# Optimization experiments

Hardware: AMD Instinct MI355X
Metric: run time of the kernel (lower is better)

Reference implementation:

```python
import jax, jax.numpy as jnp
import numpy as np

NUM_HEADS = 8
EPS = 1e-12  # torch F.normalize default eps


def conv1x1(x, w):
    # x: [b,c,h,w], w: [o,c]
    return jnp.einsum('bchw,oc->bohw', x, w)


def dwconv3x3(x, w):
    # depthwise 3x3, w: [c,1,3,3]
    return jax.lax.conv_general_dilated(
        x, w, window_strides=(1, 1), padding=((1, 1), (1, 1)),
        dimension_numbers=('NCHW', 'OIHW', 'NCHW'),
        feature_group_count=x.shape[1])


def l2norm(x):
    n = jnp.sqrt(jnp.sum(x * x, axis=-1, keepdims=True))
    return x / jnp.maximum(n, EPS)


def channel_attn(q, k, v, temperature, b, c, h, w):
    hd = c // NUM_HEADS
    q = l2norm(q.reshape(b, NUM_HEADS, hd, h * w))
    k = l2norm(k.reshape(b, NUM_HEADS, hd, h * w))
    v = v.reshape(b, NUM_HEADS, hd, h * w)
    attn = jnp.einsum('bndl,bnel->bnde', q, k) * temperature  # [b,nh,hd,hd]
    attn = jax.nn.softmax(attn, axis=-1)
    out = jnp.einsum('bnde,bnel->bndl', attn, v)
    return out.reshape(b, c, h, w)


def fdfp(x, w1, w2, h, w):
    xf = jnp.fft.rfft2(x, norm='ortho')  # over last two axes
    xfreq = jnp.concatenate([xf.real, xf.imag], axis=1)
    xfreq = conv1x1(xfreq, w1)
    xfreq = jax.nn.gelu(xfreq, approximate=False)
    xfreq = conv1x1(xfreq, w2)
    c2 = xfreq.shape[1] // 2
    xc = jax.lax.complex(xfreq[:, :c2], xfreq[:, c2:])
    return jnp.fft.irfft2(xc, s=(h, w), norm='ortho')


def setup_inputs() -> dict:
    key = jax.random.key(0)
    ks = jax.random.split(key, 10)
    dim = 192
    b, h, w = 4, 128, 128
    s = 0.05
    return {
        'x': jax.random.normal(ks[0], (b, dim, h, w), jnp.float32),
        'w_qkv1': jax.random.normal(ks[1], (3 * dim, dim), jnp.float32) * s,
        'w_qkv1_dw': jax.random.normal(ks[2], (3 * dim, 1, 3, 3), jnp.float32) * s,
        'w_proj1': jax.random.normal(ks[3], (dim, dim), jnp.float32) * s,
        'w_fdfp1': jax.random.normal(ks[4], (2 * dim, 2 * dim), jnp.float32) * s,
        'w_fdfp2': jax.random.normal(ks[5], (2 * dim, 2 * dim), jnp.float32) * s,
        'w_kv2': jax.random.normal(ks[6], (2 * dim, dim), jnp.float32) * s,
        'w_kv2_dw': jax.random.normal(ks[7], (2 * dim, 1, 3, 3), jnp.float32) * s,
        'w_proj2': jax.random.normal(ks[8], (dim, dim), jnp.float32) * s,
        'temperature': jnp.ones((NUM_HEADS, 1, 1), jnp.float32),
    }


def reference(x, w_qkv1, w_qkv1_dw, w_proj1, w_fdfp1, w_fdfp2,
              w_kv2, w_kv2_dw, w_proj2, temperature):
    b, c, h, w = x.shape
    # Stage 1: spatial-domain transposed (channel) attention
    qkv1 = dwconv3x3(conv1x1(x, w_qkv1), w_qkv1_dw)
    q1, k1, v1 = jnp.split(qkv1, 3, axis=1)
    out1 = channel_attn(q1, k1, v1, temperature, b, c, h, w)
    out1 = conv1x1(out1, w_proj1)
    # Stage 2: frequency-domain query, spatial K/V from stage-1 output
    q2 = fdfp(x, w_fdfp1, w_fdfp2, h, w)
    kv2 = dwconv3x3(conv1x1(out1, w_kv2), w_kv2_dw)
    k2, v2 = jnp.split(kv2, 2, axis=1)
    out2 = channel_attn(q2, k2, v2, temperature, b, c, h, w)
    out2 = conv1x1(out2, w_proj2)
    return out2
```

## Files before the change

kernel.cpp:

```cpp
#include <hip/hip_runtime.h>
#include <math.h>

typedef _Float16 half_t;
typedef half_t h8v __attribute__((ext_vector_type(8)));
typedef half_t h4v __attribute__((ext_vector_type(4)));
typedef float f32x4 __attribute__((ext_vector_type(4)));

namespace {
constexpr int DIMC = 192;
constexpr int NB = 4;
constexpr int HH = 128, WW = 128;
constexpr int HW = HH * WW;
constexpr int NH = 8, HD = 24;
constexpr int FP = 80;
constexpr long LT_PART = 128L * 192 * FP;
constexpr long LT_B    = 2 * LT_PART;
constexpr long LT_ROW  = 192L * FP;
constexpr long XB  = 192L * HW;
constexpr long CB0 = 0;
constexpr long CB1 = 15728640;
constexpr long OFF_T1 = 37748736;
constexpr long OFF_Q2 = 50331648;
constexpr long OFF_S  = 62914560;
constexpr long OFF_KT = 0;
constexpr long OFF_KF = 25165824;
constexpr long OFF_O2 = 0;
constexpr int  GSL = 64;
constexpr long SM_INVQ1 = OFF_S;
constexpr long SM_INVK1 = OFF_S + 768;
constexpr long SM_INVQ2 = OFF_S + 1536;
constexpr long SM_INVK2 = OFF_S + 2304;
constexpr long SM_ATT   = OFF_S + 3072;
constexpr long H0       = OFF_S + 168960;
constexpr long H_WQKV = H0;
constexpr long H_WF   = H0 + 55296;
constexpr long H_W1   = H0 + 92160;
constexpr long H_W2   = H0 + 165888;
constexpr long H_PRJ  = H0 + 239616;
constexpr long H_B2   = H0 + 258048;
constexpr long H_B3   = H0 + 290816;
constexpr long H_B1T  = H0 + 323584;
constexpr long H_B4T  = H0 + 333824;
constexpr float PI2 = 6.283185307179586476f;
}

__global__ void cvt16_k(const float* __restrict__ in, half_t* __restrict__ o, int n) {
    int i = blockIdx.x * 256 + threadIdx.x;
    if (i < n) o[i] = (half_t)in[i];
}
__global__ void initB1t_k(half_t* __restrict__ B) {
    int idx = blockIdx.x * 256 + threadIdx.x;
    if (idx >= 160 * 128) return;
    int j = idx / 128, k = idx % 128;
    float v = 0.f;
    if (j < 65) v = cosf(PI2 * ((k * j) & 127) / 128.f) * (1.f / 128.f);
    else if (j >= 80 && j < 145) v = -sinf(PI2 * ((k * (j - 80)) & 127) / 128.f) * (1.f / 128.f);
    B[idx] = (half_t)v;
}
__global__ void initB2h_k(half_t* __restrict__ B) {
    int idx = blockIdx.x * 256 + threadIdx.x;
    int m = idx >> 8, cin = idx & 255;
    int pd = m >> 7, ky = m & 127;
    int ps = cin >> 7, y = cin & 127;
    float c, s; sincosf(PI2 * ((ky * y) & 127) / 128.f, &s, &c);
    float v = (pd == 0) ? (ps == 0 ? c : s) : (ps == 0 ? -s : c);
    B[idx] = (half_t)v;
}
__global__ void initB3h_k(half_t* __restrict__ B) {
    int idx = blockIdx.x * 256 + threadIdx.x;
    int m = idx >> 8, cin = idx & 255;
    int pd = m >> 7, y = m & 127;
    int ps = cin >> 7, ky = cin & 127;
    float c, s; sincosf(PI2 * ((y * ky) & 127) / 128.f, &s, &c);
    float v = (pd == 0) ? (ps == 0 ? c : -s) : (ps == 0 ? s : c);
    B[idx] = (half_t)v;
}
__global__ void initB4t_k(half_t* __restrict__ B) {
    int idx = blockIdx.x * 256 + threadIdx.x;
    if (idx >= 128 * 160) return;
    int j = idx / 160, k = idx % 160;
    float v = 0.f;
    if (k < 80) {
        if (k == 0) v = 1.f / 128.f;
        else if (k < 64) v = 2.f * cosf(PI2 * ((k * j) & 127) / 128.f) / 128.f;
        else if (k == 64) v = cosf(PI2 * ((64 * j) & 127) / 128.f) / 128.f;
    } else {
        int kx = k - 80;
        if (kx >= 1 && kx < 64) v = -2.f * sinf(PI2 * ((kx * j) & 127) / 128.f) / 128.f;
    }
    B[idx] = (half_t)v;
}
__global__ void fusew_k(const float* __restrict__ wkv, const float* __restrict__ wproj,
                        half_t* __restrict__ wf) {
    int o = blockIdx.x, c = threadIdx.x;
    float acc = 0.f;
    for (int m = 0; m < 192; ++m) acc += wkv[o * 192 + m] * wproj[m * 192 + c];
    wf[o * 192 + c] = (half_t)acc;
}

template<int PFOLD, int GELU>
__global__ __launch_bounds__(256) void k2m(
    const half_t* __restrict__ W16, int Cin,
    const float* __restrict__ X, long xBatch, int iSplit, long iLo, long iHi,
    float* __restrict__ out, long oBatch, int oSplit, long oLo, long oHi) {
    __shared__ __align__(16) half_t Wh[64 * 40];
    __shared__ __align__(16) half_t Xh[256 * 40];
    const int t = threadIdx.x;
    const int o0 = blockIdx.x * 64;
    const long p0 = (long)blockIdx.y * 256;
    const long xb = (long)blockIdx.z * xBatch;
    const long ob = (long)blockIdx.z * oBatch;
    const int lane = t & 63, wv = t >> 6;
    const int fr = lane & 15, fg = lane >> 4;
    const int so = t >> 2, scg = (t & 3) * 8;
    f32x4 acc[4][4];
#pragma unroll
    for (int m = 0; m < 4; ++m)
#pragma unroll
        for (int n = 0; n < 4; ++n) acc[m][n] = {0.f, 0.f, 0.f, 0.f};
    long pa;
    {
        long p = p0 + t;
        if (PFOLD) { long q = p / 80; pa = q * LT_ROW + (p - q * 80); } else pa = p;
    }
    for (int k0 = 0; k0 < Cin; k0 += 32) {
        __syncthreads();
        *(h8v*)&Wh[so * 40 + scg] =
            *(const h8v*)(W16 + (long)(o0 + so) * Cin + k0 + scg);
#pragma unroll
        for (int s = 0; s < 2; ++s) {
            int cb = k0 + s * 16;
            long rb = (cb < iSplit) ? (long)cb * iLo : (long)(cb - iSplit) * iLo + iHi;
            const float* g = X + xb + rb + pa;
            float v[16];
#pragma unroll
            for (int j = 0; j < 16; ++j) v[j] = g[(long)j * iLo];
            h8v h0, h1;
#pragma unroll
            for (int j = 0; j < 8; ++j) { h0[j] = (half_t)v[j]; h1[j] = (half_t)v[8 + j]; }
            *(h8v*)&Xh[t * 40 + s * 16] = h0;
            *(h8v*)&Xh[t * 40 + s * 16 + 8] = h1;
        }
        __syncthreads();
        h8v a[4], bb[4];
#pragma unroll
        for (int m = 0; m < 4; ++m) a[m] = *(const h8v*)&Wh[(m * 16 + fr) * 40 + fg * 8];
#pragma unroll
        for (int n = 0; n < 4; ++n) bb[n] = *(const h8v*)&Xh[(wv * 64 + n * 16 + fr) * 40 + fg * 8];
#pragma unroll
        for (int m = 0; m < 4; ++m)
#pragma unroll
            for (int n = 0; n < 4; ++n)
                acc[m][n] = __builtin_amdgcn_mfma_f32_16x16x32_f16(a[m], bb[n], acc[m][n], 0, 0, 0);
    }
    long pe[4];
#pragma unroll
    for (int n = 0; n < 4; ++n) {
        long p = p0 + wv * 64 + n * 16 + fr;
        if (PFOLD) { long q = p / 80; pe[n] = q * LT_ROW + (p - q * 80); } else pe[n] = p;
    }
#pragma unroll
    for (int m = 0; m < 4; ++m)
#pragma unroll
        for (int i = 0; i < 4; ++i) {
            int o = o0 + m * 16 + fg * 4 + i;
            long oadr = ob + ((o < oSplit) ? (long)o * oLo : (long)(o - oSplit) * oLo + oHi);
#pragma unroll
            for (int n = 0; n < 4; ++n) {
                float v = acc[m][n][i];
                if (GELU) v = 0.5f * v * (1.f + erff(v * 0.70710678118654752f));
                out[oadr + pe[n]] = v;
            }
        }
}

__global__ __launch_bounds__(256) void k2big(
    const half_t* __restrict__ B16,
    const float* __restrict__ X, float* __restrict__ out) {
    __shared__ __align__(16) half_t Xh[8 * 64 * 40];
    const int t = threadIdx.x;
    const long p0 = (long)blockIdx.x * 64;
    const long xb = (long)blockIdx.y * LT_B;
    const int lane = t & 63, wv = t >> 6;
    const int fr = lane & 15, fg = lane >> 4;
    {
        const int sp = t & 63;
        const int c0 = t >> 6;
        const float* gp = X + xb + p0 + sp;
#pragma unroll 8
        for (int j = 0; j < 64; ++j) {
            int ci = c0 + j * 4;
            long rb = (ci < 128) ? (long)ci * LT_ROW : (long)(ci - 128) * LT_ROW + LT_PART;
            Xh[((ci >> 5) * 64 + sp) * 40 + (ci & 31)] = (half_t)gp[rb];
        }
    }
    __syncthreads();
    f32x4 acc[4][4];
#pragma unroll
    for (int m = 0; m < 4; ++m)
#pragma unroll
        for (int n = 0; n < 4; ++n) acc[m][n] = {0.f, 0.f, 0.f, 0.f};
    for (int k0 = 0; k0 < 256; k0 += 32) {
        const int s = k0 >> 5;
        h8v a[4], bb[4];
#pragma unroll
        for (int m = 0; m < 4; ++m)
            a[m] = *(const h8v*)(B16 + (long)(wv * 64 + m * 16 + fr) * 256 + k0 + fg * 8);
#pragma unroll
        for (int n = 0; n < 4; ++n)
            bb[n] = *(const h8v*)&Xh[(s * 64 + n * 16 + fr) * 40 + fg * 8];
#pragma unroll
        for (int m = 0; m < 4; ++m)
#pragma unroll
            for (int n = 0; n < 4; ++n)
                acc[m][n] = __builtin_amdgcn_mfma_f32_16x16x32_f16(a[m], bb[n], acc[m][n], 0, 0, 0);
    }
#pragma unroll
    for (int m = 0; m < 4; ++m)
#pragma unroll
        for (int i = 0; i < 4; ++i) {
            int o = wv * 64 + m * 16 + fg * 4 + i;
            long oadr = xb + ((o < 128) ? (long)o * LT_ROW : (long)(o - 128) * LT_ROW + LT_PART);
#pragma unroll
            for (int n = 0; n < 4; ++n)
                out[oadr + p0 + n * 16 + fr] = acc[m][n][i];
        }
}

__global__ __launch_bounds__(512) void kff4(
    const half_t* __restrict__ W1, const half_t* __restrict__ W2,
    const float* __restrict__ X, float* __restrict__ out) {
    __shared__ __align__(16) half_t S[12 * 64 * 40];
    const int t = threadIdx.x;
    const long p0 = (long)blockIdx.x * 64;
    const long xb = (long)blockIdx.y * LT_B;
    const int lane = t & 63, wv = t >> 6;
    const int fr = lane & 15, fg = lane >> 4;
    {
        const int sp = t & 63;
        const int g = t >> 6;
        long pa; { long p = p0 + sp; long q = p / 80; pa = q * LT_ROW + (p - q * 80); }
        const float* gp = X + xb + pa;
#pragma unroll
        for (int ch = 0; ch < 12; ++ch) {
            int ci0 = ch * 32 + g * 4;
            h4v h;
#pragma unroll
            for (int j = 0; j < 4; ++j) {
                int ci = ci0 + j;
                long rb = (ci < 192) ? (long)ci * 80 : (long)(ci - 192) * 80 + LT_PART;
                h[j] = (half_t)gp[rb];
            }
            *(h4v*)&S[(ch * 64 + sp) * 40 + g * 4] = h;
        }
    }
    __syncthreads();
    f32x4 acc[3][4];
#pragma unroll
    for (int m = 0; m < 3; ++m)
#pragma unroll
        for (int n = 0; n < 4; ++n) acc[m][n] = {0.f, 0.f, 0.f, 0.f};
    for (int k0 = 0; k0 < 384; k0 += 32) {
        const int s = k0 >> 5;
        h8v a[3], bb[4];
#pragma unroll
        for (int m = 0; m < 3; ++m)
            a[m] = *(const h8v*)(W1 + (long)(wv * 48 + m * 16 + fr) * 384 + k0 + fg * 8);
#pragma unroll
        for (int n = 0; n < 4; ++n)
            bb[n] = *(const h8v*)&S[(s * 64 + n * 16 + fr) * 40 + fg * 8];
#pragma unroll
        for (int m = 0; m < 3; ++m)
#pragma unroll
            for (int n = 0; n < 4; ++n)
                acc[m][n] = __builtin_amdgcn_mfma_f32_16x16x32_f16(a[m], bb[n], acc[m][n], 0, 0, 0);
    }
    __syncthreads();
#pragma unroll
    for (int m = 0; m < 3; ++m)
#pragma unroll
        for (int n = 0; n < 4; ++n) {
            int o4 = wv * 48 + m * 16 + fg * 4;
            int p = n * 16 + fr;
            h4v h;
#pragma unroll
            for (int i = 0; i < 4; ++i) {
                float v = acc[m][n][i];
                v = 0.5f * v * (1.f + erff(v * 0.70710678118654752f));
                h[i] = (half_t)v;
            }
            *(h4v*)&S[((o4 >> 5) * 64 + p) * 40 + (o4 & 31)] = h;
        }
#pragma unroll
    for (int m = 0; m < 3; ++m)
#pragma unroll
        for (int n = 0; n < 4; ++n) acc[m][n] = {0.f, 0.f, 0.f, 0.f};
    __syncthreads();
    for (int k0 = 0; k0 < 384; k0 += 32) {
        const int s = k0 >> 5;
        h8v a[3], bb[4];
#pragma unroll
        for (int m = 0; m < 3; ++m)
            a[m] = *(const h8v*)(W2 + (long)(wv * 48 + m * 16 + fr) * 384 + k0 + fg * 8);
#pragma unroll
        for (int n = 0; n < 4; ++n)
            bb[n] = *(const h8v*)&S[(s * 64 + n * 16 + fr) * 40 + fg * 8];
#pragma unroll
        for (int m = 0; m < 3; ++m)
#pragma unroll
            for (int n = 0; n < 4; ++n)
                acc[m][n] = __builtin_amdgcn_mfma_f32_16x16x32_f16(a[m], bb[n], acc[m][n], 0, 0, 0);
    }
    long pe[4];
#pragma unroll
    for (int n = 0; n < 4; ++n) {
        long p = p0 + n * 16 + fr;
        long q = p / 80; pe[n] = q * LT_ROW + (p - q * 80);
    }
#pragma unroll
    for (int m = 0; m < 3; ++m)
#pragma unroll
        for (int i = 0; i < 4; ++i) {
            int o = wv * 48 + m * 16 + fg * 4 + i;
            long oadr = xb + ((o < 192) ? (long)o * 80 : (long)(o - 192) * 80 + LT_PART);
#pragma unroll
            for (int n = 0; n < 4; ++n) out[oadr + pe[n]] = acc[m][n][i];
        }
}

template<int NF, int NORM>
__global__ __launch_bounds__(256) void k1m(
    const float* __restrict__ A, long aBatch, long aC, long aRow, int aSplit, long aHiOff, int K,
    const uint* __restrict__ Bt32,
    float* __restrict__ out, long oBatch, long oC, long oRow, int oSplit, long oHiOff,
    float* __restrict__ inv) {
    __shared__ __align__(16) half_t Ah[128 * 40];
    __shared__ __align__(16) half_t Bh[160 * 40];
    const int t = threadIdx.x;
    const long ab = (long)blockIdx.z * aBatch + (long)blockIdx.x * aC;
    const long ob = (long)blockIdx.z * oBatch + (long)blockIdx.x * oC;
    const int N = NF * 32;
    const int lane = t & 63, wv = t >> 6;
    const int wm = wv >> 1, wn = wv & 1;
    const int fr = lane & 15, fg = lane >> 4;
    const int sr = t >> 1, shalf = t & 1;
    const int Kw = K >> 1;
    f32x4 acc[4][NF];
#pragma unroll
    for (int m = 0; m < 4; ++m)
#pragma unroll
        for (int n = 0; n < NF; ++n) acc[m][n] = {0.f, 0.f, 0.f, 0.f};
    for (int k0 = 0; k0 < K; k0 += 32) {
        __syncthreads();
        {
            int cb = k0 + shalf * 16;
            long rb = (cb < aSplit) ? (long)cb : (long)(cb - aSplit) + aHiOff;
            const float* g = A + ab + (long)sr * aRow + rb;
            float4 v0 = *(const float4*)g;
            float4 v1 = *(const float4*)(g + 4);
            float4 v2 = *(const float4*)(g + 8);
            float4 v3 = *(const float4*)(g + 12);
            h8v h0, h1;
            h0[0] = (half_t)v0.x; h0[1] = (half_t)v0.y; h0[2] = (half_t)v0.z; h0[3] = (half_t)v0.w;
            h0[4] = (half_t)v1.x; h0[5] = (half_t)v1.y; h0[6] = (half_t)v1.z; h0[7] = (half_t)v1.w;
            h1[0] = (half_t)v2.x; h1[1] = (half_t)v2.y; h1[2] = (half_t)v2.z; h1[3] = (half_t)v2.w;
            h1[4] = (half_t)v3.x; h1[5] = (half_t)v3.y; h1[6] = (half_t)v3.z; h1[7] = (half_t)v3.w;
            *(h8v*)&Ah[sr * 40 + shalf * 16] = h0;
            *(h8v*)&Ah[sr * 40 + shalf * 16 + 8] = h1;
        }
        for (int j = t; j < N * 16; j += 256) {
            int n = j >> 4, kw = j & 15;
            *(uint*)&Bh[n * 40 + kw * 2] = Bt32[(long)n * Kw + (k0 >> 1) + kw];
        }
        __syncthreads();
        h8v a[4], bb[NF];
#pragma unroll
        for (int m = 0; m < 4; ++m) a[m] = *(const h8v*)&Ah[(wm * 64 + m * 16 + fr) * 40 + fg * 8];
#pragma unroll
        for (int n = 0; n < NF; ++n) bb[n] = *(const h8v*)&Bh[(wn * NF * 16 + n * 16 + fr) * 40 + fg * 8];
#pragma unroll
        for (int m = 0; m < 4; ++m)
#pragma unroll
            for (int n = 0; n < NF; ++n)
                acc[m][n] = __builtin_amdgcn_mfma_f32_16x16x32_f16(a[m], bb[n], acc[m][n], 0, 0, 0);
    }
#pragma unroll
    for (int m = 0; m < 4; ++m)
#pragma unroll
        for (int i = 0; i < 4; ++i) {
            int r = wm * 64 + m * 16 + fg * 4 + i;
            float* orow = out + ob + (long)r * oRow;
#pragma unroll
            for (int n = 0; n < NF; ++n) {
                int j = wn * NF * 16 + n * 16 + fr;
                long jm = (j < oSplit) ? (long)j : (long)(j - oSplit) + oHiOff;
                orow[jm] = acc[m][n][i];
            }
        }
    if (NORM) {
        float ss = 0.f;
#pragma unroll
        for (int m = 0; m < 4; ++m)
#pragma unroll
            for (int n = 0; n < NF; ++n)
#pragma unroll
                for (int i = 0; i < 4; ++i) ss += acc[m][n][i] * acc[m][n][i];
        __syncthreads();
        float* red = (float*)Ah;
        red[t] = ss;
        __syncthreads();
        for (int st = 128; st > 0; st >>= 1) {
            if (t < st) red[t] += red[t + st];
            __syncthreads();
        }
        if (t == 0) inv[(long)blockIdx.z * 192 + blockIdx.x] = 1.f / fmaxf(sqrtf(red[0]), 1e-12f);
    }
}

__global__ __launch_bounds__(256) void dw3_k(
    const float* __restrict__ in, long inBatch,
    const float* __restrict__ w9,
    float* __restrict__ out, long outBatch,
    int normCnt, float* __restrict__ inv) {
    const int c = blockIdx.x, b = blockIdx.y;
    const int t = threadIdx.x;
    const float* ip = in + (long)b * inBatch + (long)c * HW;
    float* op = out + (long)b * outBatch + (long)c * HW;
    const float* wp = w9 + c * 9;
    const float w0 = wp[0], w1 = wp[1], w2 = wp[2];
    const float w3 = wp[3], w4 = wp[4], w5 = wp[5];
    const float w6 = wp[6], w7 = wp[7], w8 = wp[8];
    const int tx = t & 31;
    const int x0 = tx * 4;
    const int y0 = (t >> 5) * 16;
    const bool lx = (tx > 0), rx = (tx < 31);
    float Ar[6], Br[6], Cr[6];
#define LOADROW(Y, R) do { \
        const float* _p = ip + (Y) * 128 + x0; \
        float4 _v = *(const float4*)_p; \
        R[1] = _v.x; R[2] = _v.y; R[3] = _v.z; R[4] = _v.w; \
        R[0] = lx ? _p[-1] : 0.f; \
        R[5] = rx ? _p[4] : 0.f; } while (0)
    if (y0 == 0) { Ar[0]=Ar[1]=Ar[2]=Ar[3]=Ar[4]=Ar[5]=0.f; }
    else LOADROW(y0 - 1, Ar);
    LOADROW(y0, Br);
    float ss = 0.f;
#pragma unroll
    for (int i = 0; i < 16; ++i) {
        int y = y0 + i;
        if (y + 1 < 128) { LOADROW(y + 1, Cr); }
        else { Cr[0]=Cr[1]=Cr[2]=Cr[3]=Cr[4]=Cr[5]=0.f; }
        float o0 = Ar[0]*w0 + Ar[1]*w1 + Ar[2]*w2
                 + Br[0]*w3 + Br[1]*w4 + Br[2]*w5
                 + Cr[0]*w6 + Cr[1]*w7 + Cr[2]*w8;
        float o1 = Ar[1]*w0 + Ar[2]*w1 + Ar[3]*w2
                 + Br[1]*w3 + Br[2]*w4 + Br[3]*w5
                 + Cr[1]*w6 + Cr[2]*w7 + Cr[3]*w8;
        float o2 = Ar[2]*w0 + Ar[3]*w1 + Ar[4]*w2
                 + Br[2]*w3 + Br[3]*w4 + Br[4]*w5
                 + Cr[2]*w6 + Cr[3]*w7 + Cr[4]*w8;
        float o3 = Ar[3]*w0 + Ar[4]*w1 + Ar[5]*w2
                 + Br[3]*w3 + Br[4]*w4 + Br[5]*w5
                 + Cr[3]*w6 + Cr[4]*w7 + Cr[5]*w8;
        *(float4*)(op + y * 128 + x0) = make_float4(o0, o1, o2, o3);
        ss += o0*o0 + o1*o1 + o2*o2 + o3*o3;
#pragma unroll
        for (int j = 0; j < 6; ++j) { Ar[j] = Br[j]; Br[j] = Cr[j]; }
    }
#undef LOADROW
    if (normCnt > 0 && c < normCnt) {
        __shared__ float red[256];
        red[t] = ss;
        __syncthreads();
        for (int st = 128; st > 0; st >>= 1) {
            if (t < st) red[t] += red[t + st];
            __syncthreads();
        }
        if (t == 0) inv[(long)b * 192 + c] = 1.f / fmaxf(sqrtf(red[0]), 1e-12f);
    }
}

__global__ __launch_bounds__(576) void gramf_k(
    const float* __restrict__ q, long qB,
    const float* __restrict__ k, long kB,
    float* __restrict__ gp) {
    __shared__ float qs[HD][260];
    __shared__ float ks[HD][260];
    const int bn = blockIdx.x, ls = blockIdx.y;
    const int b = bn >> 3, n = bn & 7;
    const int t = threadIdx.x;
    const int l0 = ls * 256;
    const float* qp = q + (long)b * qB + (long)(n * HD) * HW + l0;
    const float* kp = k + (long)b * kB + (long)(n * HD) * HW + l0;
    for (int idx = t; idx < HD * 64; idx += 576) {
        int row = idx >> 6, c4 = (idx & 63) * 4;
        *(float4*)&qs[row][c4] = *(const float4*)(qp + (long)row * HW + c4);
        *(float4*)&ks[row][c4] = *(const float4*)(kp + (long)row * HW + c4);
    }
    __syncthreads();
    const int d = t / 24, e = t - d * 24;
    float acc = 0.f;
#pragma unroll 8
    for (int j = 0; j < 256; j += 4) {
        float4 a = *(const float4*)&qs[d][j];
        float4 bb = *(const float4*)&ks[e][j];
        acc += a.x * bb.x + a.y * bb.y + a.z * bb.z + a.w * bb.w;
    }
    gp[((long)bn * 576 + t) * GSL + ls] = acc;
}

__global__ __launch_bounds__(256) void softmax_k(
    const float* __restrict__ gp, const float* __restrict__ invq,
    const float* __restrict__ invk, const float* __restrict__ temp,
    float* __restrict__ attn) {
    int bn = blockIdx.x;
    int b = bn >> 3, n = bn & 7;
    int t = threadIdx.x;
    __shared__ float sums[576];
    for (int idx = t; idx < 576; idx += 256) {
        const float* g = gp + ((long)bn * 576 + idx) * GSL;
        float s = 0.f;
        for (int i = 0; i < GSL; i += 4) {
            float4 v = *(const float4*)(g + i);
            s += v.x + v.y + v.z + v.w;
        }
        sums[idx] = s;
    }
    __syncthreads();
    int d = t;
    if (d >= HD) return;
    float tt = temp[n];
    float iq = invq[b * 192 + n * HD + d];
    float row[HD];
#pragma unroll
    for (int e = 0; e < HD; ++e)
        row[e] = sums[d * HD + e] * iq * invk[b * 192 + n * HD + e] * tt;
    float m = row[0];
#pragma unroll
    for (int e = 1; e < HD; ++e) m = fmaxf(m, row[e]);
    float ssum = 0.f;
#pragma unroll
    for (int e = 0; e < HD; ++e) { row[e] = expf(row[e] - m); ssum += row[e]; }
    float is = 1.f / ssum;
#pragma unroll
    for (int e = 0; e < HD; ++e) attn[(long)bn * 576 + d * HD + e] = row[e] * is;
}

__global__ void attnapply_k(const float* __restrict__ attn, const float* __restrict__ v,
                            long vB, float* __restrict__ out, long outB) {
    int p = blockIdx.x * 256 + threadIdx.x;
    int bn = blockIdx.y;
    int b = bn >> 3, n = bn & 7;
    __shared__ float a[576];
    for (int i = threadIdx.x; i < 576; i += 256) a[i] = attn[(long)bn * 576 + i];
    __syncthreads();
    const float* vp = v + (long)b * vB + (long)(n * HD) * HW + p;
    float acc[HD];
#pragma unroll
    for (int d = 0; d < HD; ++d) acc[d] = 0.f;
    for (int e = 0; e < HD; ++e) {
        float vv = vp[(long)e * HW];
#pragma unroll
        for (int d = 0; d < HD; ++d) acc[d] += a[d * HD + e] * vv;
    }
    float* op = out + (long)b * outB + (long)(n * HD) * HW + p;
#pragma unroll
    for (int d = 0; d < HD; ++d) op[(long)d * HW] = acc[d];
}

extern "C" void kernel_launch(void* const* d_in, const int* in_sizes, int n_in,
                              void* d_out, int out_size, void* d_ws, size_t ws_size,
                              hipStream_t stream) {
    const float* x        = (const float*)d_in[0];
    const float* w_qkv1   = (const float*)d_in[1];
    const float* w_qkv1dw = (const float*)d_in[2];
    const float* w_proj1  = (const float*)d_in[3];
    const float* w_fdfp1  = (const float*)d_in[4];
    const float* w_fdfp2  = (const float*)d_in[5];
    const float* w_kv2    = (const float*)d_in[6];
    const float* w_kv2dw  = (const float*)d_in[7];
    const float* w_proj2  = (const float*)d_in[8];
    const float* temp     = (const float*)d_in[9];
    float* out = (float*)d_out;
    float* ws  = (float*)d_ws;
    dim3 blk(256);
    const int BIG = 1 << 20;

    cvt16_k<<<432, blk, 0, stream>>>(w_qkv1, (half_t*)(ws + H_WQKV), 110592);
    cvt16_k<<<576, blk, 0, stream>>>(w_fdfp1, (half_t*)(ws + H_W1), 147456);
    cvt16_k<<<576, blk, 0, stream>>>(w_fdfp2, (half_t*)(ws + H_W2), 147456);
    cvt16_k<<<144, blk, 0, stream>>>(w_proj2, (half_t*)(ws + H_PRJ), 36864);
    initB1t_k<<<80, blk, 0, stream>>>((half_t*)(ws + H_B1T));
    initB2h_k<<<256, blk, 0, stream>>>((half_t*)(ws + H_B2));
    initB3h_k<<<256, blk, 0, stream>>>((half_t*)(ws + H_B3));
    initB4t_k<<<80, blk, 0, stream>>>((half_t*)(ws + H_B4T));
    fusew_k<<<384, 192, 0, stream>>>(w_kv2, w_proj1, (half_t*)(ws + H_WF));

    k1m<5, 0><<<dim3(192, 1, 4), blk, 0, stream>>>(
        x, XB, (long)HW, 128L, BIG, 0L, 128,
        (const uint*)(ws + H_B1T),
        ws + CB0, LT_B, (long)FP, LT_ROW, 80, LT_PART, nullptr);
    k2big<<<dim3(240, 4), blk, 0, stream>>>(
        (const half_t*)(ws + H_B2), ws + CB0, ws + CB1);
    kff4<<<dim3(160, 4), 512, 0, stream>>>(
        (const half_t*)(ws + H_W1), (const half_t*)(ws + H_W2),
        ws + CB1, ws + CB0);
    k2big<<<dim3(240, 4), blk, 0, stream>>>(
        (const half_t*)(ws + H_B3), ws + CB0, ws + CB1);
    k1m<4, 1><<<dim3(192, 1, 4), blk, 0, stream>>>(
        ws + CB1, LT_B, (long)FP, LT_ROW, 80, LT_PART, 160,
        (const uint*)(ws + H_B4T),
        ws + OFF_Q2, XB, (long)HW, 128L, BIG, 0L, ws + SM_INVQ2);

    for (int ch = 0; ch < 3; ++ch) {
        k2m<0, 0><<<dim3(3, 64, 4), blk, 0, stream>>>(
            (const half_t*)(ws + H_WQKV) + (long)ch * 192 * 192, 192,
            x, XB, BIG, (long)HW, 0L,
            ws + OFF_T1, XB, BIG, (long)HW, 0L);
        dw3_k<<<dim3(192, 4), blk, 0, stream>>>(
            ws + OFF_T1, XB, w_qkv1dw + ch * 192 * 9,
            ws + (long)ch * 192 * HW, (long)576 * HW,
            ch == 2 ? 0 : 192,
            ch == 0 ? ws + SM_INVQ1 : ws + SM_INVK1);
    }
    gramf_k<<<dim3(32, GSL), 576, 0, stream>>>(
        ws, (long)576 * HW, ws + (long)192 * HW, (long)576 * HW, ws + OFF_T1);
    softmax_k<<<32, blk, 0, stream>>>(ws + OFF_T1, ws + SM_INVQ1, ws + SM_INVK1, temp, ws + SM_ATT);
    attnapply_k<<<dim3(64, 32), blk, 0, stream>>>(
        ws + SM_ATT, ws + (long)384 * HW, (long)576 * HW, ws + OFF_T1, XB);

    k2m<0, 0><<<dim3(6, 64, 4), blk, 0, stream>>>(
        (const half_t*)(ws + H_WF), 192,
        ws + OFF_T1, XB, BIG, (long)HW, 0L,
        ws + OFF_KT, (long)384 * HW, BIG, (long)HW, 0L);
    dw3_k<<<dim3(384, 4), blk, 0, stream>>>(
        ws + OFF_KT, (long)384 * HW, w_kv2dw, ws + OFF_KF, (long)384 * HW,
        192, ws + SM_INVK2);

    gramf_k<<<dim3(32, GSL), 576, 0, stream>>>(
        ws + OFF_Q2, XB, ws + OFF_KF, (long)384 * HW, ws + OFF_KT);
    softmax_k<<<32, blk, 0, stream>>>(ws + OFF_KT, ws + SM_INVQ2, ws + SM_INVK2, temp, ws + SM_ATT);
    attnapply_k<<<dim3(64, 32), blk, 0, stream>>>(
        ws + SM_ATT, ws + OFF_KF + (long)192 * HW, (long)384 * HW, ws + OFF_O2, XB);
    k2m<0, 0><<<dim3(3, 64, 4), blk, 0, stream>>>(
        (const half_t*)(ws + H_PRJ), 192,
        ws + OFF_O2, XB, BIG, (long)HW, 0L,
        out, XB, BIG, (long)HW, 0L);
}
```

Baseline: 632.6 us.

## Replace 1x1-conv GEMM with full-channel tile kernel that loads input once

The generic k2m 1x1-conv kernel, which tiled output channels over the grid and re-read the input pixels once per output-channel block, is replaced by kcv. In kcv each block stages all 192 input channels for 64 pixels in shared memory once, and each wave computes 48 output channels with weights read directly from global memory. This removes the redundant input reads across output-channel blocks and the per-k-step syncthreads. The cost is smaller pixel tiles, uncached global weight loads inside the MFMA loop, and a larger shared-memory footprint per block. The 384-output case uses 8 waves.

```diff
diff --git a/kernel.cpp b/kernel.cpp
--- a/kernel.cpp
+++ b/kernel.cpp
@@ -98,79 +98,58 @@
     wf[o * 192 + c] = (half_t)acc;
 }
 
-template<int PFOLD, int GELU>
-__global__ __launch_bounds__(256) void k2m(
-    const half_t* __restrict__ W16, int Cin,
-    const float* __restrict__ X, long xBatch, int iSplit, long iLo, long iHi,
-    float* __restrict__ out, long oBatch, int oSplit, long oLo, long oHi) {
-    __shared__ __align__(16) half_t Wh[64 * 40];
-    __shared__ __align__(16) half_t Xh[256 * 40];
+template<int NW>
+__global__ __launch_bounds__(NW * 64) void kcv(
+    const half_t* __restrict__ W, const float* __restrict__ X, long xB,
+    float* __restrict__ out, long oB) {
+    __shared__ __align__(16) half_t S[6 * 64 * 40];
     const int t = threadIdx.x;
-    const int o0 = blockIdx.x * 64;
-    const long p0 = (long)blockIdx.y * 256;
-    const long xb = (long)blockIdx.z * xBatch;
-    const long ob = (long)blockIdx.z * oBatch;
+    const long p0 = (long)blockIdx.x * 64;
+    const long xb = (long)blockIdx.y * xB;
+    const long ob = (long)blockIdx.y * oB;
     const int lane = t & 63, wv = t >> 6;
     const int fr = lane & 15, fg = lane >> 4;
-    const int so = t >> 2, scg = (t & 3) * 8;
-    f32x4 acc[4][4];
-#pragma unroll
-    for (int m = 0; m < 4; ++m)
+    {
+        const int sp = t & 63;
+        const int g = t >> 6;
+        const float* gp = X + xb + p0 + sp;
+        for (int grp = g; grp < 48; grp += NW) {
+            int ci0 = grp * 4;
+            h4v h;
+#pragma unroll
+            for (int j = 0; j < 4; ++j) h[j] = (half_t)gp[(long)(ci0 + j) * HW];
+            *(h4v*)&S[((ci0 >> 5) * 64 + sp) * 40 + (ci0 & 31)] = h;
+        }
+    }
+    __syncthreads();
+    f32x4 acc[3][4];
+#pragma unroll
+    for (int m = 0; m < 3; ++m)
 #pragma unroll
         for (int n = 0; n < 4; ++n) acc[m][n] = {0.f, 0.f, 0.f, 0.f};
-    long pa;
-    {
-        long p = p0 + t;
-        if (PFOLD) { long q = p / 80; pa = q * LT_ROW + (p - q * 80); } else pa = p;
-    }
-    for (int k0 = 0; k0 < Cin; k0 += 32) {
-        __syncthreads();
-        *(h8v*)&Wh[so * 40 + scg] =
-            *(const h8v*)(W16 + (long)(o0 + so) * Cin + k0 + scg);
-#pragma unroll
-        for (int s = 0; s < 2; ++s) {
-            int cb = k0 + s * 16;
-            long rb = (cb < iSplit) ? (long)cb * iLo : (long)(cb - iSplit) * iLo + iHi;
-            const float* g = X + xb + rb + pa;
-            float v[16];
-#pragma unroll
-            for (int j = 0; j < 16; ++j) v[j] = g[(long)j * iLo];
-            h8v h0, h1;
-#pragma unroll
-            for (int j = 0; j < 8; ++j) { h0[j] = (half_t)v[j]; h1[j] = (half_t)v[8 + j]; }
-            *(h8v*)&Xh[t * 40 + s * 16] = h0;
-            *(h8v*)&Xh[t * 40 + s * 16 + 8] = h1;
-        }
-        __syncthreads();
-        h8v a[4], bb[4];
-#pragma unroll
-        for (int m = 0; m < 4; ++m) a[m] = *(const h8v*)&Wh[(m * 16 + fr) * 40 + fg * 8];
-#pragma unroll
-        for (int n = 0; n < 4; ++n) bb[n] = *(const h8v*)&Xh[(wv * 64 + n * 16 + fr) * 40 + fg * 8];
-#pragma unroll
-        for (int m = 0; m < 4; ++m)
+    for (int k0 = 0; k0 < 192; k0 += 32) {
+        const int s = k0 >> 5;
+        h8v a[3], bb[4];
+#pragma unroll
+        for (int m = 0; m < 3; ++m)
+            a[m] = *(const h8v*)(W + (long)(wv * 48 + m * 16 + fr) * 192 + k0 + fg * 8);
+#pragma unroll
+        for (int n = 0; n < 4; ++n)
+            bb[n] = *(const h8v*)&S[(s * 64 + n * 16 + fr) * 40 + fg * 8];
+#pragma unroll
+        for (int m = 0; m < 3; ++m)
 #pragma unroll
             for (int n = 0; n < 4; ++n)
                 acc[m][n] = __builtin_amdgcn_mfma_f32_16x16x32_f16(a[m], bb[n], acc[m][n], 0, 0, 0);
     }
-    long pe[4];
-#pragma unroll
-    for (int n = 0; n < 4; ++n) {
-        long p = p0 + wv * 64 + n * 16 + fr;
-        if (PFOLD) { long q = p / 80; pe[n] = q * LT_ROW + (p - q * 80); } else pe[n] = p;
-    }
-#pragma unroll
-    for (int m = 0; m < 4; ++m)
+#pragma unroll
+    for (int m = 0; m < 3; ++m)
 #pragma unroll
         for (int i = 0; i < 4; ++i) {
-            int o = o0 + m * 16 + fg * 4 + i;
-            long oadr = ob + ((o < oSplit) ? (long)o * oLo : (long)(o - oSplit) * oLo + oHi);
-#pragma unroll
-            for (int n = 0; n < 4; ++n) {
-                float v = acc[m][n][i];
-                if (GELU) v = 0.5f * v * (1.f + erff(v * 0.70710678118654752f));
-                out[oadr + pe[n]] = v;
-            }
+            int o = wv * 48 + m * 16 + fg * 4 + i;
+            float* row = out + ob + (long)o * HW + p0;
+#pragma unroll
+            for (int n = 0; n < 4; ++n) row[n * 16 + fr] = acc[m][n][i];
         }
 }
 
@@ -613,10 +592,9 @@
         ws + OFF_Q2, XB, (long)HW, 128L, BIG, 0L, ws + SM_INVQ2);
 
     for (int ch = 0; ch < 3; ++ch) {
-        k2m<0, 0><<<dim3(3, 64, 4), blk, 0, stream>>>(
-            (const half_t*)(ws + H_WQKV) + (long)ch * 192 * 192, 192,
-            x, XB, BIG, (long)HW, 0L,
-            ws + OFF_T1, XB, BIG, (long)HW, 0L);
+        kcv<4><<<dim3(256, 4), 256, 0, stream>>>(
+            (const half_t*)(ws + H_WQKV) + (long)ch * 192 * 192,
+            x, XB, ws + OFF_T1, XB);
         dw3_k<<<dim3(192, 4), blk, 0, stream>>>(
             ws + OFF_T1, XB, w_qkv1dw + ch * 192 * 9,
             ws + (long)ch * 192 * HW, (long)576 * HW,
@@ -629,10 +607,8 @@
     attnapply_k<<<dim3(64, 32), blk, 0, stream>>>(
         ws + SM_ATT, ws + (long)384 * HW, (long)576 * HW, ws + OFF_T1, XB);
 
-    k2m<0, 0><<<dim3(6, 64, 4), blk, 0, stream>>>(
-        (const half_t*)(ws + H_WF), 192,
-        ws + OFF_T1, XB, BIG, (long)HW, 0L,
-        ws + OFF_KT, (long)384 * HW, BIG, (long)HW, 0L);
+    kcv<8><<<dim3(256, 4), 512, 0, stream>>>(
+        (const half_t*)(ws + H_WF), ws + OFF_T1, XB, ws + OFF_KT, (long)384 * HW);
     dw3_k<<<dim3(384, 4), blk, 0, stream>>>(
         ws + OFF_KT, (long)384 * HW, w_kv2dw, ws + OFF_KF, (long)384 * HW,
         192, ws + SM_INVK2);
@@ -642,8 +618,6 @@
     softmax_k<<<32, blk, 0, stream>>>(ws + OFF_KT, ws + SM_INVQ2, ws + SM_INVK2, temp, ws + SM_ATT);
     attnapply_k<<<dim3(64, 32), blk, 0, stream>>>(
         ws + SM_ATT, ws + OFF_KF + (long)192 * HW, (long)384 * HW, ws + OFF_O2, XB);
-    k2m<0, 0><<<dim3(3, 64, 4), blk, 0, stream>>>(
-        (const half_t*)(ws + H_PRJ), 192,
-        ws + OFF_O2, XB, BIG, (long)HW, 0L,
-        out, XB, BIG, (long)HW, 0L);
-}
+    kcv<4><<<dim3(256, 4), 256, 0, stream>>>(
+        (const half_t*)(ws + H_PRJ), ws + OFF_O2, XB, out, XB);
+}
```

Result: faster. 578.7 us (median of 2 runs) (-8.5%).
